# Optimization experiments

Measured on AMD Instinct MI355X. Metric: run time of the kernel, lower is better.

The kernel has to match this reference:

```python
import jax, jax.numpy as jnp
import numpy as np

B, S, D = 4, 2048, 2048
H = 16
NOPE, ROPE, VD = 128, 64, 128
QK = NOPE + ROPE            # 192 per-head q/k dim
KVR = 512                   # kv_lora_rank
THETA = 10000.0
EPS = 1e-6
SCALE = QK ** -0.5


def _freqs(seq_len, d, theta):
    inv = 1.0 / (theta ** (np.arange(0, d, 2, dtype=np.float64) / d))
    ang = np.outer(np.arange(seq_len, dtype=np.float64), inv)  # [S, d//2]
    return jnp.asarray(np.cos(ang), jnp.float32), jnp.asarray(np.sin(ang), jnp.float32)


def apply_rope(x, cos, sin):
    # x: [B, S, H, d]; cos/sin: [S, d//2]; complex multiply on (even, odd) pairs
    xr = x.reshape(*x.shape[:-1], -1, 2)
    xe, xo = xr[..., 0], xr[..., 1]
    c = cos[None, :, None, :]
    s = sin[None, :, None, :]
    ye = xe * c - xo * s
    yo = xe * s + xo * c
    return jnp.stack([ye, yo], axis=-1).reshape(x.shape)


def rmsnorm(x, w, eps=EPS):
    return x * jax.lax.rsqrt(jnp.mean(x * x, axis=-1, keepdims=True) + eps) * w


def setup_inputs() -> dict:
    key = jax.random.key(0)
    ks = jax.random.split(key, 6)
    sd = 0.02
    x = jax.random.normal(ks[0], (B, S, D), jnp.float32)
    wq = jax.random.normal(ks[1], (H * QK, D), jnp.float32) * sd
    wkv_a = jax.random.normal(ks[2], (KVR + ROPE, D), jnp.float32) * sd
    kv_norm_w = jnp.ones((KVR,), jnp.float32)
    wkv_b = jax.random.normal(ks[3], (H * (NOPE + VD), KVR), jnp.float32) * sd
    wo = jax.random.normal(ks[4], (D, H * VD), jnp.float32) * sd
    cos, sin = _freqs(S, ROPE, THETA)
    return {"x": x, "wq": wq, "wkv_a": wkv_a, "kv_norm_w": kv_norm_w,
            "wkv_b": wkv_b, "wo": wo, "freqs_cos": cos, "freqs_sin": sin}


def reference(x, wq, wkv_a, kv_norm_w, wkv_b, wo, freqs_cos, freqs_sin):
    b, s, _ = x.shape
    # query projection (q_lora_rank == 0 path)
    q = jnp.einsum('bsd,ed->bse', x, wq).reshape(b, s, H, QK)
    q_nope, q_pe = q[..., :NOPE], q[..., NOPE:]
    q_pe = apply_rope(q_pe, freqs_cos, freqs_sin)

    # low-rank KV latent + decoupled rope key
    kv = jnp.einsum('bsd,ed->bse', x, wkv_a)          # [b,s,KVR+ROPE]
    kv_c, k_pe = kv[..., :KVR], kv[..., KVR:]
    k_pe = apply_rope(k_pe[:, :, None, :], freqs_cos, freqs_sin)  # [b,s,1,ROPE]
    kv_c = rmsnorm(kv_c, kv_norm_w)
    kvb = jnp.einsum('bsr,er->bse', kv_c, wkv_b).reshape(b, s, H, NOPE + VD)
    k_nope, v = kvb[..., :NOPE], kvb[..., NOPE:]
    k = jnp.concatenate([k_nope, jnp.broadcast_to(k_pe, (b, s, H, ROPE))], axis=-1)
    q_full = jnp.concatenate([q_nope, q_pe], axis=-1)

    # causal attention
    scores = jnp.einsum('bqhd,bkhd->bhqk', q_full, k) * SCALE
    mask = jnp.triu(jnp.full((s, s), -jnp.inf, jnp.float32), k=1)
    scores = scores + mask[None, None]
    p = jax.nn.softmax(scores, axis=-1)
    out = jnp.einsum('bhqk,bkhd->bqhd', p, v).reshape(b, s, H * VD)
    return jnp.einsum('bse,de->bsd', out, wo)
```

## Files before the change

kernel.cpp:

```cpp
#include <hip/hip_runtime.h>
#include <math.h>

#define BB 4
#define SS 2048
#define DD 2048
#define HH 16
#define NOPE 128
#define ROPE 64
#define VD 128
#define QKD 192
#define KVR 512
#define NP1 3712
#define ROWS (BB*SS)
#define SCL2 0.1041216338380858f

typedef __attribute__((ext_vector_type(8))) short bf16x8;
typedef __attribute__((ext_vector_type(4))) float f32x4;
typedef unsigned short bfu;
typedef __attribute__((address_space(1))) const void GV;
typedef __attribute__((address_space(3))) void LV;

__device__ __forceinline__ float bf2f(unsigned int u) {
    unsigned int i = u << 16; float f; __builtin_memcpy(&f, &i, 4); return f;
}
__device__ __forceinline__ unsigned int f2bf(float f) {
    unsigned int i; __builtin_memcpy(&i, &f, 4);
    return (i + 0x7fffu + ((i >> 16) & 1u)) >> 16;
}
__device__ __forceinline__ unsigned int cvt_pk_bf16(float lo, float hi) {
    unsigned int r;
    asm("v_cvt_pk_bf16_f32 %0, %1, %2" : "=v"(r) : "v"(lo), "v"(hi));
    return r;
}

__global__ void cast_f32_bf16(const float* __restrict__ src, bfu* __restrict__ dst,
                              long n_src, long n_dst) {
    long i = (long)blockIdx.x * blockDim.x + threadIdx.x;
    if (i * 4 >= n_dst) return;
    unsigned int lo = 0, hi = 0;
    if (i * 4 < n_src) {
        float4 v = ((const float4*)src)[i];
        lo = f2bf(v.x) | (f2bf(v.y) << 16);
        hi = f2bf(v.z) | (f2bf(v.w) << 16);
    }
    ((uint2*)dst)[i] = make_uint2(lo, hi);
}

__global__ void cast_weights(const float* __restrict__ wq, const float* __restrict__ wa,
                             const float* __restrict__ wb, const float* __restrict__ wo,
                             bfu* __restrict__ dq, bfu* __restrict__ da,
                             bfu* __restrict__ db, bfu* __restrict__ dwo) {
    long i = (long)blockIdx.x * 256 + threadIdx.x;
    const float* src; bfu* dst; long off, n_src; float scl = 1.0f;
    if (i < 1572864L)        { src = wq; dst = dq;  off = i;            n_src = 1572864L; scl = SCL2; }
    else if (i < 1900544L)   { src = wa; dst = da;  off = i - 1572864L; n_src = 294912L;  }
    else if (i < 2424832L)   { src = wb; dst = db;  off = i - 1900544L; n_src = 524288L;  }
    else if (i < 3473408L)   { src = wo; dst = dwo; off = i - 2424832L; n_src = 1048576L; }
    else return;
    unsigned int lo = 0, hi = 0;
    if (off < n_src) {
        float4 v = ((const float4*)src)[off];
        lo = f2bf(v.x * scl) | (f2bf(v.y * scl) << 16);
        hi = f2bf(v.z * scl) | (f2bf(v.w * scl) << 16);
    }
    ((uint2*)dst)[off] = make_uint2(lo, hi);
}

template <int MODE>
__global__ void __launch_bounds__(256)
gemm_bt(const bfu* __restrict__ A, const bfu* __restrict__ Bt,
        void* __restrict__ Cv, bfu* __restrict__ C2, int N, int K) {
    __shared__ __align__(16) char lds[32768];
    char* AsB = lds;
    char* BsB = lds + 16384;
    const int tid  = threadIdx.x;
    const int lane = tid & 63;
    const int wid  = tid >> 6;
    const int wr   = wid >> 1, wc = wid & 1;
    const long m0 = (long)blockIdx.y * 128;
    const long n0 = (long)blockIdx.x * 128;

    f32x4 acc[4][4] = {};

    const int lr = lane >> 3;
    const int SB = (lane & 7) << 4;

    for (int k0 = 0; k0 < K; k0 += 64) {
        __syncthreads();
#pragma unroll
        for (int i = 0; i < 4; ++i) {
            int rb = wid * 32 + i * 8;
            int R  = rb + lr;
            int c  = (SB ^ ((R & 7) << 4)) >> 1;
            const bfu* gA = A  + (m0 + R) * (long)K + k0 + c;
            const bfu* gB = Bt + (n0 + R) * (long)K + k0 + c;
            __builtin_amdgcn_global_load_lds((GV*)gA, (LV*)(AsB + rb * 128), 16, 0, 0);
            __builtin_amdgcn_global_load_lds((GV*)gB, (LV*)(BsB + rb * 128), 16, 0, 0);
        }
        __syncthreads();
#pragma unroll
        for (int kk = 0; kk < 2; ++kk) {
            bf16x8 av[4], bv[4];
            const int cb = kk * 64 + ((lane >> 4) << 4);
#pragma unroll
            for (int m = 0; m < 4; ++m) {
                int R = wr * 64 + m * 16 + (lane & 15);
                av[m] = *(const bf16x8*)(AsB + R * 128 + (cb ^ ((R & 7) << 4)));
            }
#pragma unroll
            for (int n = 0; n < 4; ++n) {
                int R = wc * 64 + n * 16 + (lane & 15);
                bv[n] = *(const bf16x8*)(BsB + R * 128 + (cb ^ ((R & 7) << 4)));
            }
#pragma unroll
            for (int m = 0; m < 4; ++m)
#pragma unroll
                for (int n = 0; n < 4; ++n)
                    acc[m][n] = __builtin_amdgcn_mfma_f32_16x16x32_bf16(av[m], bv[n], acc[m][n], 0, 0, 0);
        }
    }

    const int cr = (lane >> 4) << 2;
    const int cc = lane & 15;
#pragma unroll
    for (int m = 0; m < 4; ++m)
#pragma unroll
        for (int n = 0; n < 4; ++n)
#pragma unroll
            for (int r = 0; r < 4; ++r) {
                long row = m0 + wr * 64 + m * 16 + cr + r;
                long col = n0 + wc * 64 + n * 16 + cc;
                float val = acc[m][n][r];
                if (MODE == 1) {
                    ((float*)Cv)[row * N + col] = val;
                } else if (MODE == 0) {
                    ((bfu*)Cv)[row * N + col] = (bfu)f2bf(val);
                } else {
                    long b_ = row >> 11;
                    long s  = row & 2047;
                    long h  = col >> 8;
                    long wi = col & 255;
                    if (wi < 128)
                        C2[((b_ * HH + h) * SS + s) * (long)QKD + wi] = (bfu)f2bf(val);
                    else
                        ((bfu*)Cv)[row * 2048 + h * 128 + (wi - 128)] = (bfu)f2bf(val);
                }
            }
}

__global__ void rope_q(const bfu* __restrict__ p1, bfu* __restrict__ qr,
                       const float* __restrict__ fc, const float* __restrict__ fs) {
    long t = (long)blockIdx.x * 256 + threadIdx.x;
    int  ch = (int)(t % 24);
    long r  = t / 24;
    int  s  = (int)(r & 2047);
    long bh = r >> 11;
    long b_ = bh >> 4;
    int  h  = (int)(bh & 15);
    const bfu* src = p1 + (b_ * SS + s) * (long)NP1 + h * QKD + ch * 8;
    bfu* dst = qr + (bh * SS + s) * (long)QKD + ch * 8;
    bf16x8 v = *(const bf16x8*)src;
    if (ch >= 16) {
        int i0 = (ch - 16) * 4;
        unsigned int out[4];
#pragma unroll
        for (int k = 0; k < 4; ++k) {
            float e = bf2f((unsigned short)v[2 * k]);
            float o = bf2f((unsigned short)v[2 * k + 1]);
            float c = fc[s * 32 + i0 + k], sn = fs[s * 32 + i0 + k];
            out[k] = cvt_pk_bf16(e * c - o * sn, e * sn + o * c);
        }
        uint4 u = make_uint4(out[0], out[1], out[2], out[3]);
        *(uint4*)dst = u;
    } else {
        *(bf16x8*)dst = v;
    }
}

__global__ void __launch_bounds__(256)
rms_rope_kv(const bfu* __restrict__ p1, const float* __restrict__ wn,
            bfu* __restrict__ kvc, bfu* __restrict__ kpe,
            const float* __restrict__ fc, const float* __restrict__ fs) {
    const int row = blockIdx.x;
    const int t   = threadIdx.x;
    const int s   = row & (SS - 1);
    const long base = (long)row * NP1 + 3072;
    unsigned int v = *(const unsigned int*)(p1 + base + 2 * t);
    float a = bf2f(v & 0xffff), c2 = bf2f(v >> 16);
    float ssum = a * a + c2 * c2;
#pragma unroll
    for (int d = 1; d < 64; d <<= 1) ssum += __shfl_xor(ssum, d);
    __shared__ float red[4];
    const int lane = t & 63, w = t >> 6;
    if (lane == 0) red[w] = ssum;
    __syncthreads();
    float tot = red[0] + red[1] + red[2] + red[3];
    float scale = rsqrtf(tot * (1.0f / 512.0f) + 1e-6f);
    float w0 = wn[2 * t], w1 = wn[2 * t + 1];
    unsigned int out = f2bf(a * scale * w0) | (f2bf(c2 * scale * w1) << 16);
    *(unsigned int*)(kvc + (long)row * KVR + 2 * t) = out;
    if (t < 32) {
        unsigned int pv = *(const unsigned int*)(p1 + base + KVR + 2 * t);
        float e = bf2f(pv & 0xffff), o = bf2f(pv >> 16);
        float cc = fc[s * 32 + t], sn = fs[s * 32 + t];
        unsigned int po = f2bf(e * cc - o * sn) | (f2bf(e * sn + o * cc) << 16);
        *(unsigned int*)(kpe + (long)row * ROPE + 2 * t) = po;
    }
}

__global__ void pe_fill(const bfu* __restrict__ kpe, bfu* __restrict__ kall) {
    long t = (long)blockIdx.x * 256 + threadIdx.x;
    int  ch = (int)(t & 7);
    long r  = t >> 3;
    int  s  = (int)(r & 2047);
    long bh = r >> 11;
    long b_ = bh >> 4;
    bf16x8 v = *(const bf16x8*)(kpe + (b_ * SS + s) * (long)ROPE + ch * 8);
    *(bf16x8*)(kall + (bh * SS + s) * (long)QKD + NOPE + ch * 8) = v;
}

__global__ void __launch_bounds__(256)
transpose_v2(const bfu* __restrict__ vpack, bfu* __restrict__ vt) {
    __shared__ __align__(16) char tile[64 * 256];
    const int tid = threadIdx.x;
    const int bid = blockIdx.x;
    const int st  = bid & 31;
    const int bh  = bid >> 5;
    const int h   = bh & 15;
    const long b_ = bh >> 4;
    const long sbase = b_ * SS + st * 64;
#pragma unroll
    for (int i = 0; i < 4; ++i) {
        int idx = i * 256 + tid;
        int row = idx >> 4;
        int ch  = (idx & 15) ^ ((row >> 3) & 7);
        const bfu* src = vpack + (sbase + row) * 2048 + h * 128 + ch * 8;
        __builtin_amdgcn_global_load_lds((GV*)src, (LV*)(tile + idx * 16), 16, 0, 0);
    }
    __syncthreads();
#pragma unroll
    for (int i = 0; i < 4; ++i) {
        int idx = i * 256 + tid;
        int sc = idx & 7;
        int v  = (idx >> 3) & 127;
        bfu tmp[8];
#pragma unroll
        for (int k = 0; k < 8; ++k) {
            int row = sc * 8 + k;
            tmp[k] = *(const bfu*)(tile + row * 256 + (((v >> 3) ^ ((row >> 3) & 7)) << 4) + (v & 7) * 2);
        }
        *(bf16x8*)(vt + ((long)bh * VD + v) * SS + st * 64 + sc * 8) = *(bf16x8*)tmp;
    }
}

__device__ __forceinline__ void attn_tile64(
    const char* kbuf, const char* vbuf, char* pw,
    const bf16x8 (&qf)[6], f32x4 (&accv)[8],
    float& ms, float& ls, int kv0, int qa, int ql, int kg, int lane) {
    f32x4 sc[4] = {};
#pragma unroll
    for (int j = 0; j < 4; ++j)
#pragma unroll
        for (int d = 0; d < 6; ++d) {
            int row  = j * 16 + ql;
            int slot = (d * 4 + kg) ^ (ql & 7);
            bf16x8 kf = *(const bf16x8*)(kbuf + row * 384 + slot * 16);
            sc[j] = __builtin_amdgcn_mfma_f32_16x16x32_bf16(kf, qf[d], sc[j], 0, 0, 0);
        }
    float p[4][4];
    float mx = -1e30f;
#pragma unroll
    for (int j = 0; j < 4; ++j)
#pragma unroll
        for (int r = 0; r < 4; ++r) {
            float s = sc[j][r];
            int kv = kv0 + j * 16 + kg * 4 + r;
            s = (kv > qa) ? -1e30f : s;
            p[j][r] = s;
            mx = fmaxf(mx, s);
        }
    mx = fmaxf(mx, __shfl_xor(mx, 16));
    mx = fmaxf(mx, __shfl_xor(mx, 32));
    float rs = 0.f;
    if (__all(mx <= ms)) {
#pragma unroll
        for (int j = 0; j < 4; ++j)
#pragma unroll
            for (int r = 0; r < 4; ++r) {
                float e = exp2f(p[j][r] - ms);
                p[j][r] = e;
                rs += e;
            }
        rs += __shfl_xor(rs, 16);
        rs += __shfl_xor(rs, 32);
        ls += rs;
    } else {
        float mn = fmaxf(ms, mx);
        float al = exp2f(ms - mn);
        ms = mn;
#pragma unroll
        for (int j = 0; j < 4; ++j)
#pragma unroll
            for (int r = 0; r < 4; ++r) {
                float e = exp2f(p[j][r] - mn);
                p[j][r] = e;
                rs += e;
            }
        rs += __shfl_xor(rs, 16);
        rs += __shfl_xor(rs, 32);
        ls = ls * al + rs;
        float alT[4];
#pragma unroll
        for (int r = 0; r < 4; ++r)
            alT[r] = __shfl(al, (lane & 48) + kg * 4 + r);
#pragma unroll
        for (int v8 = 0; v8 < 8; ++v8)
#pragma unroll
            for (int r = 0; r < 4; ++r)
                accv[v8][r] *= alT[r];
    }
#pragma unroll
    for (int j = 0; j < 4; ++j) {
        uint2 u;
        u.x = cvt_pk_bf16(p[j][0], p[j][1]);
        u.y = cvt_pk_bf16(p[j][2], p[j][3]);
        int slot = (2 * j + (kg >> 1)) ^ (ql & 7);
        *(uint2*)(pw + ql * 128 + slot * 16 + (kg & 1) * 8) = u;
    }
    asm volatile("s_waitcnt lgkmcnt(0)" ::: "memory");
#pragma unroll
    for (int t2 = 0; t2 < 2; ++t2) {
        int ps = (t2 * 4 + kg) ^ (ql & 7);
        bf16x8 pa = *(const bf16x8*)(pw + ql * 128 + ps * 16);
#pragma unroll
        for (int v8 = 0; v8 < 8; ++v8) {
            int vrow = v8 * 16 + ql;
            int vs   = (t2 * 4 + kg) ^ (ql & 7);
            bf16x8 vf = *(const bf16x8*)(vbuf + vrow * 128 + vs * 16);
            accv[v8] = __builtin_amdgcn_mfma_f32_16x16x32_bf16(pa, vf, accv[v8], 0, 0, 0);
        }
    }
}

__global__ void __launch_bounds__(512)
attn(const bfu* __restrict__ qr, const bfu* __restrict__ kall,
     const bfu* __restrict__ vt, bfu* __restrict__ ao) {
    __shared__ __align__(16) char kbuf[64 * 384];
    __shared__ __align__(16) char vbuf[128 * 128];
    __shared__ __align__(16) char pbuf[8][2048];
    const int tid  = threadIdx.x;
    const int lane = tid & 63;
    const int w    = tid >> 6;
    const int ql   = lane & 15;
    const int kg   = lane >> 4;
    const int bid  = blockIdx.x;
    const int qb   = 15 - (bid >> 6);
    const int bh   = bid & 63;
    const int h    = bh & 15;
    const int b    = bh >> 4;
    const char* Q  = (const char*)(qr + (long)bh * SS * QKD);
    const char* Kp = (const char*)(kall + (long)bh * SS * QKD);
    const char* Vp = (const char*)(vt + (long)bh * VD * SS);
    char* pw = pbuf[w];

    const int qa_min = qb * 128 + w * 16;
    const int qa = qa_min + ql;

    bf16x8 qf[6];
#pragma unroll
    for (int d = 0; d < 6; ++d)
        qf[d] = *(const bf16x8*)(Q + (long)(qa_min + ql) * 384 + d * 64 + kg * 16);

    f32x4 accv[8] = {};
    float ms = -1e30f, ls = 0.f;
    const int ntiles = 2 * qb + 2;

    for (int t = 0; t < ntiles; ++t) {
        const int kv0 = t * 64;
        __syncthreads();
#pragma unroll
        for (int i = 0; i < 3; ++i) {
            int idx  = i * 512 + tid;
            int row  = idx / 24;
            int slot = idx - row * 24;
            int ss   = slot ^ (row & 7);
            const char* src = Kp + (long)(kv0 + row) * 384 + ss * 16;
            __builtin_amdgcn_global_load_lds((GV*)src, (LV*)(kbuf + idx * 16), 16, 0, 0);
        }
#pragma unroll
        for (int i = 0; i < 2; ++i) {
            int idx  = i * 512 + tid;
            int row  = idx >> 3;
            int slot = idx & 7;
            int ss   = slot ^ (row & 7);
            const char* src = Vp + (long)row * (SS * 2) + kv0 * 2 + ss * 16;
            __builtin_amdgcn_global_load_lds((GV*)src, (LV*)(vbuf + idx * 16), 16, 0, 0);
        }
        __syncthreads();
        if (kv0 <= qa_min + 15)
            attn_tile64(kbuf, vbuf, pw, qf, accv, ms, ls, kv0, qa, ql, kg, lane);
    }
    float li[4];
#pragma unroll
    for (int r = 0; r < 4; ++r)
        li[r] = 1.0f / __shfl(ls, (lane & 48) + kg * 4 + r);
#pragma unroll
    for (int v8 = 0; v8 < 8; ++v8)
#pragma unroll
        for (int r = 0; r < 4; ++r) {
            float o = accv[v8][r] * li[r];
            long row = (long)b * SS + qa_min + kg * 4 + r;
            ao[row * (long)(HH * VD) + h * VD + v8 * 16 + ql] = (bfu)f2bf(o);
        }
}

#define O_XB   0L
#define O_WQ   33554432L
#define O_WA   46137344L
#define O_WB   48758784L
#define O_WO   52953088L
#define O_P1   61341696L
#define O_QR   122159104L
#define O_KVC  172490752L
#define O_KPE  180879360L
#define O_AO   181927936L
#define WS_NEED 215482368L

extern "C" void kernel_launch(void* const* d_in, const int* in_sizes, int n_in,
                              void* d_out, int out_size, void* d_ws, size_t ws_size,
                              hipStream_t stream) {
    const float* x      = (const float*)d_in[0];
    const float* wq     = (const float*)d_in[1];
    const float* wkv_a  = (const float*)d_in[2];
    const float* kvnw   = (const float*)d_in[3];
    const float* wkv_b  = (const float*)d_in[4];
    const float* wo     = (const float*)d_in[5];
    const float* fcos   = (const float*)d_in[6];
    const float* fsin   = (const float*)d_in[7];
    if (ws_size < (size_t)WS_NEED) return;

    char* ws = (char*)d_ws;
    bfu* xb   = (bfu*)(ws + O_XB);
    bfu* wqb  = (bfu*)(ws + O_WQ);
    bfu* wab  = (bfu*)(ws + O_WA);
    bfu* wbb  = (bfu*)(ws + O_WB);
    bfu* wob  = (bfu*)(ws + O_WO);
    bfu* p1   = (bfu*)(ws + O_P1);
    bfu* qr   = (bfu*)(ws + O_QR);
    bfu* kvc  = (bfu*)(ws + O_KVC);
    bfu* kpe  = (bfu*)(ws + O_KPE);
    bfu* ao   = (bfu*)(ws + O_AO);
    bfu* kall = p1;
    bfu* vt   = xb;
    bfu* vpack = (bfu*)d_out;

    cast_f32_bf16<<<16384, 256, 0, stream>>>(x, xb, 16777216L, 16777216L);
    cast_weights<<<13568, 256, 0, stream>>>(wq, wkv_a, wkv_b, wo, wqb, wab, wbb, wob);

    gemm_bt<0><<<dim3(29, 64), 256, 0, stream>>>(xb, wqb, p1, nullptr, NP1, DD);

    rope_q<<<12288, 256, 0, stream>>>(p1, qr, fcos, fsin);
    rms_rope_kv<<<ROWS, 256, 0, stream>>>(p1, kvnw, kvc, kpe, fcos, fsin);

    gemm_bt<2><<<dim3(32, 64), 256, 0, stream>>>(kvc, wbb, vpack, kall, HH * 256, KVR);

    pe_fill<<<4096, 256, 0, stream>>>(kpe, kall);
    transpose_v2<<<2048, 256, 0, stream>>>(vpack, vt);

    attn<<<1024, 512, 0, stream>>>(qr, kall, vt, ao);

    gemm_bt<1><<<dim3(16, 64), 256, 0, stream>>>(ao, wob, d_out, nullptr, DD, HH * VD);
}
```

Baseline: 524.8 us.

## Scatter Q directly from projection GEMM, fuse rope with pe_fill, swizzle tiles, skip masks

The first projection GEMM now writes Q straight into the per-head [b,h,s,192] layout and the KV latent into a compact 640-wide buffer. This removes the separate rope_q copy pass over the full projection output. Q-rope is applied in place and merged with the K-pe broadcast into one kernel. Workgroup indices in the GEMM are swizzled to improve L2 locality, and the attention kernel skips the causal mask on fully visible tiles. The trade-off is scattered, uncoalesced GEMM epilogue stores with an integer divide by 192.

```diff
diff --git a/kernel.cpp b/kernel.cpp
--- a/kernel.cpp
+++ b/kernel.cpp
@@ -77,8 +77,11 @@
     const int lane = tid & 63;
     const int wid  = tid >> 6;
     const int wr   = wid >> 1, wc = wid & 1;
-    const long m0 = (long)blockIdx.y * 128;
-    const long n0 = (long)blockIdx.x * 128;
+    const int nwg  = gridDim.x * gridDim.y;
+    const int flat = blockIdx.y * gridDim.x + blockIdx.x;
+    const int swz  = (flat & 7) * (nwg >> 3) + (flat >> 3);
+    const long m0 = (long)(swz / gridDim.x) * 128;
+    const long n0 = (long)(swz % gridDim.x) * 128;
 
     f32x4 acc[4][4] = {};
 
@@ -133,9 +136,7 @@
                 float val = acc[m][n][r];
                 if (MODE == 1) {
                     ((float*)Cv)[row * N + col] = val;
-                } else if (MODE == 0) {
-                    ((bfu*)Cv)[row * N + col] = (bfu)f2bf(val);
-                } else {
+                } else if (MODE == 2) {
                     long b_ = row >> 11;
                     long s  = row & 2047;
                     long h  = col >> 8;
@@ -144,24 +145,33 @@
                         C2[((b_ * HH + h) * SS + s) * (long)QKD + wi] = (bfu)f2bf(val);
                     else
                         ((bfu*)Cv)[row * 2048 + h * 128 + (wi - 128)] = (bfu)f2bf(val);
+                } else {
+                    long b_ = row >> 11;
+                    long s  = row & 2047;
+                    if (col < 3072) {
+                        unsigned int h = (unsigned int)col / 192u;
+                        unsigned int d = (unsigned int)col - h * 192u;
+                        ((bfu*)Cv)[((b_ * HH + h) * SS + s) * (long)QKD + d] = (bfu)f2bf(val);
+                    } else {
+                        C2[row * 640 + (col - 3072)] = (bfu)f2bf(val);
+                    }
                 }
             }
 }
 
-__global__ void rope_q(const bfu* __restrict__ p1, bfu* __restrict__ qr,
-                       const float* __restrict__ fc, const float* __restrict__ fs) {
+__global__ void rope_pe_fill(bfu* __restrict__ qr, const bfu* __restrict__ kpe,
+                             bfu* __restrict__ kall,
+                             const float* __restrict__ fc, const float* __restrict__ fs) {
     long t = (long)blockIdx.x * 256 + threadIdx.x;
-    int  ch = (int)(t % 24);
-    long r  = t / 24;
+    int  ch = (int)(t & 7);
+    long r  = t >> 3;
     int  s  = (int)(r & 2047);
-    long bh = r >> 11;
+    long bh = (r >> 11) & 63;
     long b_ = bh >> 4;
-    int  h  = (int)(bh & 15);
-    const bfu* src = p1 + (b_ * SS + s) * (long)NP1 + h * QKD + ch * 8;
-    bfu* dst = qr + (bh * SS + s) * (long)QKD + ch * 8;
-    bf16x8 v = *(const bf16x8*)src;
-    if (ch >= 16) {
-        int i0 = (ch - 16) * 4;
+    if (t < 1048576L) {
+        bfu* p = qr + (bh * SS + s) * (long)QKD + NOPE + ch * 8;
+        bf16x8 v = *(const bf16x8*)p;
+        int i0 = ch * 4;
         unsigned int out[4];
 #pragma unroll
         for (int k = 0; k < 4; ++k) {
@@ -170,22 +180,22 @@
             float c = fc[s * 32 + i0 + k], sn = fs[s * 32 + i0 + k];
             out[k] = cvt_pk_bf16(e * c - o * sn, e * sn + o * c);
         }
-        uint4 u = make_uint4(out[0], out[1], out[2], out[3]);
-        *(uint4*)dst = u;
+        *(uint4*)p = make_uint4(out[0], out[1], out[2], out[3]);
     } else {
-        *(bf16x8*)dst = v;
+        bf16x8 v = *(const bf16x8*)(kpe + (b_ * SS + s) * (long)ROPE + ch * 8);
+        *(bf16x8*)(kall + (bh * SS + s) * (long)QKD + NOPE + ch * 8) = v;
     }
 }
 
 __global__ void __launch_bounds__(256)
-rms_rope_kv(const bfu* __restrict__ p1, const float* __restrict__ wn,
+rms_rope_kv(const bfu* __restrict__ kv1, const float* __restrict__ wn,
             bfu* __restrict__ kvc, bfu* __restrict__ kpe,
             const float* __restrict__ fc, const float* __restrict__ fs) {
     const int row = blockIdx.x;
     const int t   = threadIdx.x;
     const int s   = row & (SS - 1);
-    const long base = (long)row * NP1 + 3072;
-    unsigned int v = *(const unsigned int*)(p1 + base + 2 * t);
+    const long base = (long)row * 640;
+    unsigned int v = *(const unsigned int*)(kv1 + base + 2 * t);
     float a = bf2f(v & 0xffff), c2 = bf2f(v >> 16);
     float ssum = a * a + c2 * c2;
 #pragma unroll
@@ -200,23 +210,12 @@
     unsigned int out = f2bf(a * scale * w0) | (f2bf(c2 * scale * w1) << 16);
     *(unsigned int*)(kvc + (long)row * KVR + 2 * t) = out;
     if (t < 32) {
-        unsigned int pv = *(const unsigned int*)(p1 + base + KVR + 2 * t);
+        unsigned int pv = *(const unsigned int*)(kv1 + base + KVR + 2 * t);
         float e = bf2f(pv & 0xffff), o = bf2f(pv >> 16);
         float cc = fc[s * 32 + t], sn = fs[s * 32 + t];
         unsigned int po = f2bf(e * cc - o * sn) | (f2bf(e * sn + o * cc) << 16);
         *(unsigned int*)(kpe + (long)row * ROPE + 2 * t) = po;
     }
-}
-
-__global__ void pe_fill(const bfu* __restrict__ kpe, bfu* __restrict__ kall) {
-    long t = (long)blockIdx.x * 256 + threadIdx.x;
-    int  ch = (int)(t & 7);
-    long r  = t >> 3;
-    int  s  = (int)(r & 2047);
-    long bh = r >> 11;
-    long b_ = bh >> 4;
-    bf16x8 v = *(const bf16x8*)(kpe + (b_ * SS + s) * (long)ROPE + ch * 8);
-    *(bf16x8*)(kall + (bh * SS + s) * (long)QKD + NOPE + ch * 8) = v;
 }
 
 __global__ void __launch_bounds__(256)
@@ -253,6 +252,7 @@
     }
 }
 
+template <bool MASKED>
 __device__ __forceinline__ void attn_tile64(
     const char* kbuf, const char* vbuf, char* pw,
     const bf16x8 (&qf)[6], f32x4 (&accv)[8],
@@ -274,8 +274,10 @@
 #pragma unroll
         for (int r = 0; r < 4; ++r) {
             float s = sc[j][r];
-            int kv = kv0 + j * 16 + kg * 4 + r;
-            s = (kv > qa) ? -1e30f : s;
+            if (MASKED) {
+                int kv = kv0 + j * 16 + kg * 4 + r;
+                s = (kv > qa) ? -1e30f : s;
+            }
             p[j][r] = s;
             mx = fmaxf(mx, s);
         }
@@ -397,8 +399,10 @@
             __builtin_amdgcn_global_load_lds((GV*)src, (LV*)(vbuf + idx * 16), 16, 0, 0);
         }
         __syncthreads();
-        if (kv0 <= qa_min + 15)
-            attn_tile64(kbuf, vbuf, pw, qf, accv, ms, ls, kv0, qa, ql, kg, lane);
+        if (kv0 + 63 <= qa_min)
+            attn_tile64<false>(kbuf, vbuf, pw, qf, accv, ms, ls, kv0, qa, ql, kg, lane);
+        else if (kv0 <= qa_min + 15)
+            attn_tile64<true>(kbuf, vbuf, pw, qf, accv, ms, ls, kv0, qa, ql, kg, lane);
     }
     float li[4];
 #pragma unroll
@@ -419,7 +423,8 @@
 #define O_WA   46137344L
 #define O_WB   48758784L
 #define O_WO   52953088L
-#define O_P1   61341696L
+#define O_KALL 61341696L
+#define O_KV1  111673344L
 #define O_QR   122159104L
 #define O_KVC  172490752L
 #define O_KPE  180879360L
@@ -442,29 +447,28 @@
     char* ws = (char*)d_ws;
     bfu* xb   = (bfu*)(ws + O_XB);
     bfu* wqb  = (bfu*)(ws + O_WQ);
-    bfu* wab  = (bfu*)(ws + O_WA);
     bfu* wbb  = (bfu*)(ws + O_WB);
     bfu* wob  = (bfu*)(ws + O_WO);
-    bfu* p1   = (bfu*)(ws + O_P1);
+    bfu* kall = (bfu*)(ws + O_KALL);
+    bfu* kv1  = (bfu*)(ws + O_KV1);
     bfu* qr   = (bfu*)(ws + O_QR);
     bfu* kvc  = (bfu*)(ws + O_KVC);
     bfu* kpe  = (bfu*)(ws + O_KPE);
     bfu* ao   = (bfu*)(ws + O_AO);
-    bfu* kall = p1;
+    bfu* wab  = (bfu*)(ws + O_WA);
     bfu* vt   = xb;
     bfu* vpack = (bfu*)d_out;
 
     cast_f32_bf16<<<16384, 256, 0, stream>>>(x, xb, 16777216L, 16777216L);
     cast_weights<<<13568, 256, 0, stream>>>(wq, wkv_a, wkv_b, wo, wqb, wab, wbb, wob);
 
-    gemm_bt<0><<<dim3(29, 64), 256, 0, stream>>>(xb, wqb, p1, nullptr, NP1, DD);
-
-    rope_q<<<12288, 256, 0, stream>>>(p1, qr, fcos, fsin);
-    rms_rope_kv<<<ROWS, 256, 0, stream>>>(p1, kvnw, kvc, kpe, fcos, fsin);
+    gemm_bt<3><<<dim3(29, 64), 256, 0, stream>>>(xb, wqb, qr, kv1, NP1, DD);
+
+    rms_rope_kv<<<ROWS, 256, 0, stream>>>(kv1, kvnw, kvc, kpe, fcos, fsin);
 
     gemm_bt<2><<<dim3(32, 64), 256, 0, stream>>>(kvc, wbb, vpack, kall, HH * 256, KVR);
 
-    pe_fill<<<4096, 256, 0, stream>>>(kpe, kall);
+    rope_pe_fill<<<8192, 256, 0, stream>>>(qr, kpe, kall, fcos, fsin);
     transpose_v2<<<2048, 256, 0, stream>>>(vpack, vt);
 
     attn<<<1024, 512, 0, stream>>>(qr, kall, vt, ao);
```

New measurement: 511.7 us. -2.5%, faster.
